# Kernel optimization log

Measured on AMD Instinct MI355X. Metric: run time of the kernel, lower is better.

## Reference

```python
import jax, jax.numpy as jnp
import numpy as np

B, NUM_GENES, F = 8, 20000, 128
N, E, H = 50000, 800000, 128


def setup_inputs() -> dict:
    key = jax.random.key(0)
    k = jax.random.split(key, 8)
    gene_emb = jax.random.normal(k[0], (B, NUM_GENES, F), dtype=jnp.float32)
    W1 = jax.random.normal(k[1], (F, H), dtype=jnp.float32) * 0.05
    b1 = jnp.zeros((H,), dtype=jnp.float32)
    W2 = jax.random.normal(k[2], (H, H), dtype=jnp.float32) * 0.05
    b2 = jnp.zeros((H,), dtype=jnp.float32)
    global_ids = jax.random.randint(k[3], (N,), 0, NUM_GENES, dtype=jnp.int64)
    edge_index = jax.random.randint(k[4], (2, E), 0, N, dtype=jnp.int64)
    return {"gene_emb": gene_emb, "W1": W1, "b1": b1, "W2": W2, "b2": b2,
            "global_ids": global_ids, "edge_index": edge_index}


def reference(gene_emb, W1, b1, W2, b2, global_ids, edge_index):
    n = global_ids.shape[0]
    # GCN normalization with self-loops (PyG GCNConv default):
    # A_hat = A + I, deg over target nodes, norm = d^{-1/2}[src] * d^{-1/2}[dst]
    loop = jnp.arange(n)
    src = jnp.concatenate([edge_index[0], loop])  # [E+N]
    dst = jnp.concatenate([edge_index[1], loop])  # [E+N]
    deg = jnp.zeros((n,), gene_emb.dtype).at[dst].add(1.0)
    dinv = jax.lax.rsqrt(deg)  # deg >= 1 thanks to self-loops
    norm = (dinv[src] * dinv[dst])[None, :, None]  # [1, E+N, 1]

    def gcn(x, W, b):
        h = x @ W                                   # [B, N, H] transform first (linear commutes)
        msg = h[:, src, :] * norm                   # gather + scale: [B, E+N, H]
        agg = jnp.zeros_like(h).at[:, dst].add(msg)  # scatter-add over targets
        return agg + b

    x = gene_emb[:, global_ids, :]                  # [B, N, F] node feature gather
    x = jax.nn.relu(gcn(x, W1, b1))
    x = gcn(x, W2, b2)
    # global_mean_pool: each batch replica is one whole graph -> mean over nodes
    return x.mean(axis=1)                           # [B, H]
```

## Files before the change

### kernel.cpp

```cpp
#include <hip/hip_runtime.h>

#define NG 20000
#define BB 8
#define FD 128

typedef unsigned int uint;
typedef unsigned short ushort;
typedef __attribute__((ext_vector_type(8))) short short8v;
typedef __attribute__((ext_vector_type(4))) float float4v;
typedef __attribute__((ext_vector_type(4))) int int4v;
typedef __attribute__((ext_vector_type(2))) float f2v;

__device__ f2v llvm_rbl_v2f32(int4v srsrc, int voffset, int soffset, int aux)
    __asm("llvm.amdgcn.raw.buffer.load.v2f32");

__device__ __forceinline__ int4v make_srsrc(const void* p) {
    int4v r;
    r.x = (int)(uint)(uintptr_t)p;
    r.y = (int)(uint)((uintptr_t)p >> 32);
    r.z = -1;
    r.w = 0x00020000;
    return r;
}

__device__ __forceinline__ ushort f2bf(float x) {
    uint u = __float_as_uint(x);
    u += 0x7FFFu + ((u >> 16) & 1u);
    return (ushort)(u >> 16);
}
__device__ __forceinline__ float bf_lo(uint u) { return __uint_as_float(u << 16); }
__device__ __forceinline__ float bf_hi(uint u) { return __uint_as_float(u & 0xFFFF0000u); }

__global__ void k_setup(int4* csrz, int zn4, int* ideg, float* s_acc,
                        const float* __restrict__ W1, ushort* w1t, int N) {
    int i = blockIdx.x * blockDim.x + threadIdx.x;
    if (i < zn4) csrz[i] = make_int4(0, 0, 0, 0);
    if (i < N) ideg[i] = 0;
    if (i < BB * FD) s_acc[i] = 0.0f;
    if (i < FD * FD) {
        int j = i >> 7, k = i & 127;
        w1t[i] = f2bf(W1[k * 128 + j]);
    }
}

__global__ void k_count(const int* __restrict__ dst, int* ideg, int E) {
    int e = blockIdx.x * blockDim.x + threadIdx.x;
    if (e < E) atomicAdd(&ideg[dst[e]], 1);
}

__global__ void k_scanA(const int* __restrict__ ideg, float* dinv, float* cval,
                        float* wself, int* padcnt, int* offs, int* bsums, int N) {
    __shared__ int sd[256];
    int t = threadIdx.x, idx = blockIdx.x * 256 + t;
    int v = 0;
    if (idx < N) {
        int d = ideg[idx] + 1;
        float fd = (float)d;
        dinv[idx]  = rsqrtf(fd);
        float iv = 1.0f / fd;
        cval[idx]  = iv;
        wself[idx] = iv;
        v = (d + 7) & ~7;
        padcnt[idx] = v;
    }
    sd[t] = v; __syncthreads();
    for (int o = 1; o < 256; o <<= 1) {
        int x = (t >= o) ? sd[t - o] : 0;
        __syncthreads();
        sd[t] += x;
        __syncthreads();
    }
    if (idx < N) offs[idx] = sd[t] - v;
    if (t == 255) bsums[blockIdx.x] = sd[255];
}

__global__ void k_scan2(int* bsums, int nb) {
    __shared__ int sd[256];
    int t = threadIdx.x;
    int v = (t < nb) ? bsums[t] : 0;
    sd[t] = v; __syncthreads();
    for (int o = 1; o < 256; o <<= 1) {
        int x = (t >= o) ? sd[t - o] : 0;
        __syncthreads();
        sd[t] += x;
        __syncthreads();
    }
    if (t < nb) bsums[t] = sd[t] - v;
}

__global__ void k_scanB(int* offs, const int* __restrict__ bsums,
                        const int* __restrict__ gid, const float* __restrict__ wself,
                        int* cursor, int2* csr, int N) {
    int i = blockIdx.x * blockDim.x + threadIdx.x;
    if (i < N) {
        int o = offs[i] + bsums[blockIdx.x];
        offs[i] = o;
        csr[o] = make_int2(gid[i], __float_as_int(wself[i]));
        cursor[i] = 1;
    }
}

__global__ __launch_bounds__(256, 3)
void k_fillh(const int* __restrict__ src, const int* __restrict__ dst,
             const int* __restrict__ gid, const float* __restrict__ dinv,
             float* cval, const int* __restrict__ offs, int* cursor,
             int2* csr, int E, int eb,
             const float* __restrict__ gene, const ushort* __restrict__ w1t,
             uint* __restrict__ h2u) {
    __shared__ __align__(16) char smem[49152];
    if ((int)blockIdx.x < eb) {
        int e = blockIdx.x * 256 + threadIdx.x;
        if (e >= E) return;
        int s = src[e], d = dst[e];
        float nrm = dinv[s] * dinv[d];
        atomicAdd(&cval[s], nrm);
        int pos = atomicAdd(&cursor[d], 1);
        csr[offs[d] + pos] = make_int2(gid[s], __float_as_int(nrm));
        return;
    }
    ushort* Al = (ushort*)smem;
    ushort* Bl = (ushort*)(smem + 16384);
    float*  Cl = (float*)smem;
    int t = threadIdx.x;
    int hb   = blockIdx.x - eb;
    int p    = hb & 3;
    int tile = hb >> 2;
    int g0   = tile * 32;

#pragma unroll
    for (int s = 0; s < 8; s++) {
        int f = t + s * 256;
        int r = f >> 5, k0 = (f & 31) * 4;
        int bb = 2 * p + (r >> 5);
        int gg = g0 + (r & 31);
        float4 v = *(const float4*)(gene + ((size_t)bb * NG + gg) * 128 + k0);
        ushort4 u;
        u.x = f2bf(v.x); u.y = f2bf(v.y); u.z = f2bf(v.z); u.w = f2bf(v.w);
        int byte = (r * 256 + k0 * 2) ^ ((r & 7) << 4);
        *(ushort4*)((char*)Al + byte) = u;
    }
#pragma unroll
    for (int s = 0; s < 8; s++) {
        int f = t + s * 256;
        int j = f >> 4, k0 = (f & 15) * 8;
        uint4 v = *(const uint4*)(w1t + j * 128 + k0);
        int byte = (j * 256 + k0 * 2) ^ ((j & 7) << 4);
        *(uint4*)((char*)Bl + byte) = v;
    }
    __syncthreads();

    int wid = t >> 6, lane = t & 63;
    int r0 = wid * 16;
    int lrow = lane & 15, lhi = lane >> 4;
    float4v acc[8];
#pragma unroll
    for (int nf = 0; nf < 8; nf++) acc[nf] = (float4v)(0.f);

#pragma unroll
    for (int c = 0; c < 4; c++) {
        int ra = r0 + lrow;
        int byteA = (ra * 256 + (c * 32 + lhi * 8) * 2) ^ ((ra & 7) << 4);
        short8v a = *(short8v*)((char*)Al + byteA);
#pragma unroll
        for (int nf = 0; nf < 8; nf++) {
            int jb = nf * 16 + lrow;
            int byteB = (jb * 256 + (c * 32 + lhi * 8) * 2) ^ ((jb & 7) << 4);
            short8v b = *(short8v*)((char*)Bl + byteB);
            acc[nf] = __builtin_amdgcn_mfma_f32_16x16x32_bf16(a, b, acc[nf], 0, 0, 0);
        }
    }
    __syncthreads();

#pragma unroll
    for (int nf = 0; nf < 8; nf++) {
#pragma unroll
        for (int q = 0; q < 4; q++) {
            Cl[(r0 + lhi * 4 + q) * 128 + nf * 16 + lrow] = acc[nf][q];
        }
    }
    __syncthreads();

#pragma unroll
    for (int s = 0; s < 16; s++) {
        int flat = t + s * 256;
        int gi = flat >> 7, cc = flat & 127;
        float lo = Cl[gi * 128 + cc];
        float hi = Cl[(32 + gi) * 128 + cc];
        uint u = (uint)f2bf(lo) | ((uint)f2bf(hi) << 16);
        h2u[((size_t)p * NG + g0 + gi) * 128 + cc] = u;
    }
}

__global__ __launch_bounds__(512)
void k_aggp(const uint* __restrict__ hp, const int2* __restrict__ csr,
            const int* __restrict__ offs, const int* __restrict__ padcnt,
            const float* __restrict__ cval, const float* __restrict__ b1,
            float* __restrict__ s_acc, int N, int npw) {
    int p    = blockIdx.x & 3;
    int wid  = threadIdx.x >> 6, lane = threadIdx.x & 63;
    int w    = __builtin_amdgcn_readfirstlane((blockIdx.x >> 2) * 8 + wid);
    int4v sr = make_srsrc(hp + (size_t)p * NG * 128);
    int voff = lane * 8;
    int l2 = lane * 2;
    float bx = b1[l2], by = b1[l2 + 1];
    float sx0 = 0.f, sx1 = 0.f, sy0 = 0.f, sy1 = 0.f;

    int i0 = w * npw;
    int i1 = min(N, i0 + npw);
    for (int i = i0; i < i1; ++i) {
        int   e  = offs[i];
        int   pc = padcnt[i];
        float cv = cval[i];
        float ax0 = 0.f, ax1 = 0.f, ay0 = 0.f, ay1 = 0.f;
        for (int q = 0; q < pc; q += 8) {
            int ee = e + q;
            int2 c0 = csr[ee],     c1 = csr[ee + 1], c2 = csr[ee + 2], c3 = csr[ee + 3];
            int2 c4 = csr[ee + 4], c5 = csr[ee + 5], c6 = csr[ee + 6], c7 = csr[ee + 7];
            f2v u0 = llvm_rbl_v2f32(sr, voff, c0.x << 9, 0);
            f2v u1 = llvm_rbl_v2f32(sr, voff, c1.x << 9, 0);
            f2v u2 = llvm_rbl_v2f32(sr, voff, c2.x << 9, 0);
            f2v u3 = llvm_rbl_v2f32(sr, voff, c3.x << 9, 0);
            f2v u4 = llvm_rbl_v2f32(sr, voff, c4.x << 9, 0);
            f2v u5 = llvm_rbl_v2f32(sr, voff, c5.x << 9, 0);
            f2v u6 = llvm_rbl_v2f32(sr, voff, c6.x << 9, 0);
            f2v u7 = llvm_rbl_v2f32(sr, voff, c7.x << 9, 0);
            float n0 = __int_as_float(c0.y), n1 = __int_as_float(c1.y);
            float n2 = __int_as_float(c2.y), n3 = __int_as_float(c3.y);
            float n4 = __int_as_float(c4.y), n5 = __int_as_float(c5.y);
            float n6 = __int_as_float(c6.y), n7 = __int_as_float(c7.y);
            uint a, b;
            a = __float_as_uint(u0.x); b = __float_as_uint(u0.y);
            ax0 = fmaf(n0, bf_lo(a), ax0); ax1 = fmaf(n0, bf_hi(a), ax1);
            ay0 = fmaf(n0, bf_lo(b), ay0); ay1 = fmaf(n0, bf_hi(b), ay1);
            a = __float_as_uint(u1.x); b = __float_as_uint(u1.y);
            ax0 = fmaf(n1, bf_lo(a), ax0); ax1 = fmaf(n1, bf_hi(a), ax1);
            ay0 = fmaf(n1, bf_lo(b), ay0); ay1 = fmaf(n1, bf_hi(b), ay1);
            a = __float_as_uint(u2.x); b = __float_as_uint(u2.y);
            ax0 = fmaf(n2, bf_lo(a), ax0); ax1 = fmaf(n2, bf_hi(a), ax1);
            ay0 = fmaf(n2, bf_lo(b), ay0); ay1 = fmaf(n2, bf_hi(b), ay1);
            a = __float_as_uint(u3.x); b = __float_as_uint(u3.y);
            ax0 = fmaf(n3, bf_lo(a), ax0); ax1 = fmaf(n3, bf_hi(a), ax1);
            ay0 = fmaf(n3, bf_lo(b), ay0); ay1 = fmaf(n3, bf_hi(b), ay1);
            a = __float_as_uint(u4.x); b = __float_as_uint(u4.y);
            ax0 = fmaf(n4, bf_lo(a), ax0); ax1 = fmaf(n4, bf_hi(a), ax1);
            ay0 = fmaf(n4, bf_lo(b), ay0); ay1 = fmaf(n4, bf_hi(b), ay1);
            a = __float_as_uint(u5.x); b = __float_as_uint(u5.y);
            ax0 = fmaf(n5, bf_lo(a), ax0); ax1 = fmaf(n5, bf_hi(a), ax1);
            ay0 = fmaf(n5, bf_lo(b), ay0); ay1 = fmaf(n5, bf_hi(b), ay1);
            a = __float_as_uint(u6.x); b = __float_as_uint(u6.y);
            ax0 = fmaf(n6, bf_lo(a), ax0); ax1 = fmaf(n6, bf_hi(a), ax1);
            ay0 = fmaf(n6, bf_lo(b), ay0); ay1 = fmaf(n6, bf_hi(b), ay1);
            a = __float_as_uint(u7.x); b = __float_as_uint(u7.y);
            ax0 = fmaf(n7, bf_lo(a), ax0); ax1 = fmaf(n7, bf_hi(a), ax1);
            ay0 = fmaf(n7, bf_lo(b), ay0); ay1 = fmaf(n7, bf_hi(b), ay1);
        }
        sx0 += cv * fmaxf(ax0 + bx, 0.f);
        sx1 += cv * fmaxf(ax1 + bx, 0.f);
        sy0 += cv * fmaxf(ay0 + by, 0.f);
        sy1 += cv * fmaxf(ay1 + by, 0.f);
    }

    __shared__ float red[8][256];
    red[wid][lane * 4 + 0] = sx0;
    red[wid][lane * 4 + 1] = sx1;
    red[wid][lane * 4 + 2] = sy0;
    red[wid][lane * 4 + 3] = sy1;
    __syncthreads();
    int t = threadIdx.x;
    if (t < 256) {
        float s = 0.f;
#pragma unroll
        for (int wv = 0; wv < 8; wv++) s += red[wv][t];
        int l = t >> 2, c = t & 3;
        atomicAdd(&s_acc[(2 * p + (c & 1)) * 128 + 2 * l + (c >> 1)], s);
    }
}

__global__ void k_final(const float* __restrict__ s_acc, const float* __restrict__ W2,
                        const float* __restrict__ b2, float* __restrict__ out, float invN) {
    __shared__ float ss[1024];
    int t = threadIdx.x;
    for (int idx = t; idx < 1024; idx += 128) ss[idx] = s_acc[idx];
    __syncthreads();
    float acc[8];
#pragma unroll
    for (int b = 0; b < 8; b++) acc[b] = 0.f;
    for (int k = 0; k < 128; k++) {
        float w = W2[k * 128 + t];
#pragma unroll
        for (int b = 0; b < 8; b++) acc[b] += ss[b * 128 + k] * w;
    }
    float bb = b2[t];
#pragma unroll
    for (int b = 0; b < 8; b++) out[b * 128 + t] = acc[b] * invN + bb;
}


extern "C" void kernel_launch(void* const* d_in, const int* in_sizes, int n_in,
                              void* d_out, int out_size, void* d_ws, size_t ws_size,
                              hipStream_t stream) {
    const float* gene = (const float*)d_in[0];
    const float* W1   = (const float*)d_in[1];
    const float* b1   = (const float*)d_in[2];
    const float* W2   = (const float*)d_in[3];
    const float* b2   = (const float*)d_in[4];
    const int*   gid  = (const int*)d_in[5];
    const int*   eidx = (const int*)d_in[6];
    int N = in_sizes[5];
    int E = in_sizes[6] / 2;
    const int* src = eidx;
    const int* dst = eidx + E;
    float* out = (float*)d_out;

    char* p = (char*)d_ws;
    auto alloc = [&](size_t bytes) -> char* {
        char* r = p; p += (bytes + 255) & ~(size_t)255; return r;
    };
    size_t csr_cap = (size_t)E + 8 * (size_t)N;
    int*   ideg   = (int*)  alloc((size_t)N * 4);
    float* dinv   = (float*)alloc((size_t)N * 4);
    float* cval   = (float*)alloc((size_t)N * 4);
    float* wself  = (float*)alloc((size_t)N * 4);
    int*   padcnt = (int*)  alloc((size_t)N * 4);
    int*   offs   = (int*)  alloc((size_t)N * 4);
    int*   cursor = (int*)  alloc((size_t)N * 4);
    int*   bsums  = (int*)  alloc(256 * 4);
    int2*  csr    = (int2*) alloc(csr_cap * 8);
    float* s_acc  = (float*)alloc(1024 * 4);
    uint*  h2     = (uint*) alloc((size_t)NG * BB * FD * 2);
    ushort* w1t   = (ushort*)alloc(128 * 128 * 2);

    int nb = (N + 255) / 256;
    int eb = (E + 255) / 256;
    int zn4 = (int)(csr_cap * 8 / 16);
    int zb  = (zn4 + 255) / 256;
    int hblk = 4 * (NG / 32);

    const int NBLK = 2048;
    int wavesPerPair = (NBLK / 4) * 8;
    int npw = (N + wavesPerPair - 1) / wavesPerPair;

    k_setup<<<zb, 256, 0, stream>>>((int4*)csr, zn4, ideg, s_acc, W1, w1t, N);
    k_count<<<eb, 256, 0, stream>>>(dst, ideg, E);
    k_scanA<<<nb, 256, 0, stream>>>(ideg, dinv, cval, wself, padcnt, offs, bsums, N);
    k_scan2<<<1, 256, 0, stream>>>(bsums, nb);
    k_scanB<<<nb, 256, 0, stream>>>(offs, bsums, gid, wself, cursor, csr, N);
    k_fillh<<<eb + hblk, 256, 0, stream>>>(src, dst, gid, dinv, cval, offs, cursor,
                                           csr, E, eb, gene, w1t, h2);
    k_aggp <<<NBLK, 512, 0, stream>>>(h2, csr, offs, padcnt,
                                      cval, b1, s_acc, N, npw);
    k_final<<<1, 128, 0, stream>>>(s_acc, W2, b2, out, 1.0f / (float)N);
}
```

Measured before the change: 306.6 us.

## Fuse CSR build phases into one persistent kernel with grid barriers

Merges count, scan, scan-add, and edge-fill kernels into a single persistent kernel of 256 blocks that uses atomic grid barriers between phases. The remaining 256 blocks run the X@W1 MFMA tiles in a grid-stride loop concurrently with the graph build. The full CSR zero-fill is replaced by zeroing only the padding slots per node, and the s_acc atomics are spread over 8 replicas that k_final sums. The aim is to cut launch overhead, the large memset, and atomic contention. The cost is spin-wait barriers that rely on all 512 blocks being co-resident.

```diff
diff --git a/kernel.cpp b/kernel.cpp
--- a/kernel.cpp
+++ b/kernel.cpp
@@ -3,6 +3,8 @@
 #define NG 20000
 #define BB 8
 #define FD 128
+#define NBT 512
+#define NBS 256
 
 typedef unsigned int uint;
 typedef unsigned short ushort;
@@ -31,163 +33,168 @@
 __device__ __forceinline__ float bf_lo(uint u) { return __uint_as_float(u << 16); }
 __device__ __forceinline__ float bf_hi(uint u) { return __uint_as_float(u & 0xFFFF0000u); }
 
-__global__ void k_setup(int4* csrz, int zn4, int* ideg, float* s_acc,
+__global__ void k_setup(int* ideg, float* s_acc, uint* bar,
                         const float* __restrict__ W1, ushort* w1t, int N) {
     int i = blockIdx.x * blockDim.x + threadIdx.x;
-    if (i < zn4) csrz[i] = make_int4(0, 0, 0, 0);
     if (i < N) ideg[i] = 0;
-    if (i < BB * FD) s_acc[i] = 0.0f;
+    if (i < 8 * BB * FD) s_acc[i] = 0.0f;
+    if (i < 4) bar[i] = 0u;
     if (i < FD * FD) {
         int j = i >> 7, k = i & 127;
         w1t[i] = f2bf(W1[k * 128 + j]);
     }
 }
 
-__global__ void k_count(const int* __restrict__ dst, int* ideg, int E) {
-    int e = blockIdx.x * blockDim.x + threadIdx.x;
-    if (e < E) atomicAdd(&ideg[dst[e]], 1);
-}
-
-__global__ void k_scanA(const int* __restrict__ ideg, float* dinv, float* cval,
-                        float* wself, int* padcnt, int* offs, int* bsums, int N) {
-    __shared__ int sd[256];
-    int t = threadIdx.x, idx = blockIdx.x * 256 + t;
-    int v = 0;
-    if (idx < N) {
-        int d = ideg[idx] + 1;
-        float fd = (float)d;
-        dinv[idx]  = rsqrtf(fd);
-        float iv = 1.0f / fd;
-        cval[idx]  = iv;
-        wself[idx] = iv;
-        v = (d + 7) & ~7;
-        padcnt[idx] = v;
-    }
-    sd[t] = v; __syncthreads();
-    for (int o = 1; o < 256; o <<= 1) {
-        int x = (t >= o) ? sd[t - o] : 0;
-        __syncthreads();
-        sd[t] += x;
-        __syncthreads();
-    }
-    if (idx < N) offs[idx] = sd[t] - v;
-    if (t == 255) bsums[blockIdx.x] = sd[255];
-}
-
-__global__ void k_scan2(int* bsums, int nb) {
-    __shared__ int sd[256];
-    int t = threadIdx.x;
-    int v = (t < nb) ? bsums[t] : 0;
-    sd[t] = v; __syncthreads();
-    for (int o = 1; o < 256; o <<= 1) {
-        int x = (t >= o) ? sd[t - o] : 0;
-        __syncthreads();
-        sd[t] += x;
-        __syncthreads();
-    }
-    if (t < nb) bsums[t] = sd[t] - v;
-}
-
-__global__ void k_scanB(int* offs, const int* __restrict__ bsums,
-                        const int* __restrict__ gid, const float* __restrict__ wself,
-                        int* cursor, int2* csr, int N) {
-    int i = blockIdx.x * blockDim.x + threadIdx.x;
-    if (i < N) {
-        int o = offs[i] + bsums[blockIdx.x];
-        offs[i] = o;
-        csr[o] = make_int2(gid[i], __float_as_int(wself[i]));
-        cursor[i] = 1;
-    }
-}
-
-__global__ __launch_bounds__(256, 3)
-void k_fillh(const int* __restrict__ src, const int* __restrict__ dst,
-             const int* __restrict__ gid, const float* __restrict__ dinv,
-             float* cval, const int* __restrict__ offs, int* cursor,
-             int2* csr, int E, int eb,
+__device__ __forceinline__ void gbar(uint* bar, int ph) {
+    __syncthreads();
+    if (threadIdx.x == 0) {
+        __threadfence();
+        atomicAdd(&bar[ph], 1u);
+        while (atomicAdd(&bar[ph], 0u) < (uint)NBS) __builtin_amdgcn_s_sleep(4);
+    }
+    __syncthreads();
+    __threadfence();
+}
+
+__global__ __launch_bounds__(256)
+void k_build(const int* __restrict__ src, const int* __restrict__ dst,
+             const int* __restrict__ gid, int E, int N, int nb,
+             int* ideg, float* dinv, float* cval, int* padcnt, int* offs,
+             int* cursor, int2* csr, int* bsums, uint* bar,
              const float* __restrict__ gene, const ushort* __restrict__ w1t,
              uint* __restrict__ h2u) {
     __shared__ __align__(16) char smem[49152];
-    if ((int)blockIdx.x < eb) {
-        int e = blockIdx.x * 256 + threadIdx.x;
-        if (e >= E) return;
-        int s = src[e], d = dst[e];
-        float nrm = dinv[s] * dinv[d];
+    int bid = blockIdx.x, t = threadIdx.x;
+
+    if (bid >= NBS) {
+        ushort* Al = (ushort*)smem;
+        ushort* Bl = (ushort*)(smem + 16384);
+        float*  Cl = (float*)smem;
+        int ntile = 4 * (NG / 32);
+        for (int tile = bid - NBS; tile < ntile; tile += (NBT - NBS)) {
+            int p = tile & 3, g0 = (tile >> 2) * 32;
+#pragma unroll
+            for (int s = 0; s < 8; s++) {
+                int f = t + s * 256;
+                int r = f >> 5, k0 = (f & 31) * 4;
+                int bb = 2 * p + (r >> 5);
+                int gg = g0 + (r & 31);
+                float4 v = *(const float4*)(gene + ((size_t)bb * NG + gg) * 128 + k0);
+                ushort4 u;
+                u.x = f2bf(v.x); u.y = f2bf(v.y); u.z = f2bf(v.z); u.w = f2bf(v.w);
+                int byte = (r * 256 + k0 * 2) ^ ((r & 7) << 4);
+                *(ushort4*)((char*)Al + byte) = u;
+            }
+#pragma unroll
+            for (int s = 0; s < 8; s++) {
+                int f = t + s * 256;
+                int j = f >> 4, k0 = (f & 15) * 8;
+                uint4 v = *(const uint4*)(w1t + j * 128 + k0);
+                int byte = (j * 256 + k0 * 2) ^ ((j & 7) << 4);
+                *(uint4*)((char*)Bl + byte) = v;
+            }
+            __syncthreads();
+
+            int wid = t >> 6, lane = t & 63;
+            int r0 = wid * 16;
+            int lrow = lane & 15, lhi = lane >> 4;
+            float4v acc[8];
+#pragma unroll
+            for (int nf = 0; nf < 8; nf++) acc[nf] = (float4v)(0.f);
+#pragma unroll
+            for (int c = 0; c < 4; c++) {
+                int ra = r0 + lrow;
+                int byteA = (ra * 256 + (c * 32 + lhi * 8) * 2) ^ ((ra & 7) << 4);
+                short8v a = *(short8v*)((char*)Al + byteA);
+#pragma unroll
+                for (int nf = 0; nf < 8; nf++) {
+                    int jb = nf * 16 + lrow;
+                    int byteB = (jb * 256 + (c * 32 + lhi * 8) * 2) ^ ((jb & 7) << 4);
+                    short8v b = *(short8v*)((char*)Bl + byteB);
+                    acc[nf] = __builtin_amdgcn_mfma_f32_16x16x32_bf16(a, b, acc[nf], 0, 0, 0);
+                }
+            }
+            __syncthreads();
+#pragma unroll
+            for (int nf = 0; nf < 8; nf++) {
+#pragma unroll
+                for (int q = 0; q < 4; q++) {
+                    Cl[(r0 + lhi * 4 + q) * 128 + nf * 16 + lrow] = acc[nf][q];
+                }
+            }
+            __syncthreads();
+#pragma unroll
+            for (int s = 0; s < 16; s++) {
+                int flat = t + s * 256;
+                int gi = flat >> 7, cc = flat & 127;
+                float lo = Cl[gi * 128 + cc];
+                float hi = Cl[(32 + gi) * 128 + cc];
+                uint u = (uint)f2bf(lo) | ((uint)f2bf(hi) << 16);
+                h2u[((size_t)p * NG + g0 + gi) * 128 + cc] = u;
+            }
+            __syncthreads();
+        }
+        return;
+    }
+
+    int* sd = (int*)smem;
+
+    for (int e = bid * 256 + t; e < E; e += NBS * 256)
+        atomicAdd(&ideg[dst[e]], 1);
+    gbar(bar, 0);
+
+    int idx = bid * 256 + t;
+    int v = 0, d = 0, off_part = 0;
+    float iv = 0.f;
+    if (bid < nb) {
+        if (idx < N) {
+            d = ideg[idx] + 1;
+            float fd = (float)d;
+            dinv[idx] = rsqrtf(fd);
+            iv = 1.0f / fd;
+            cval[idx] = iv;
+            v = (d + 7) & ~7;
+            padcnt[idx] = v;
+        }
+        sd[t] = v; __syncthreads();
+        for (int o = 1; o < 256; o <<= 1) {
+            int x = (t >= o) ? sd[t - o] : 0;
+            __syncthreads();
+            sd[t] += x;
+            __syncthreads();
+        }
+        off_part = sd[t] - v;
+        if (t == 255) bsums[bid] = sd[255];
+    }
+    gbar(bar, 1);
+
+    if (bid < nb) {
+        int v2 = (t < nb) ? bsums[t] : 0;
+        __syncthreads();
+        sd[t] = v2; __syncthreads();
+        for (int o = 1; o < 256; o <<= 1) {
+            int x = (t >= o) ? sd[t - o] : 0;
+            __syncthreads();
+            sd[t] += x;
+            __syncthreads();
+        }
+        int prefix = (bid > 0) ? sd[bid - 1] : 0;
+        if (idx < N) {
+            int o = off_part + prefix;
+            offs[idx] = o;
+            csr[o] = make_int2(gid[idx], __float_as_int(iv));
+            cursor[idx] = 1;
+            for (int z = d; z < v; z++) csr[o + z] = make_int2(0, 0);
+        }
+    }
+    gbar(bar, 2);
+
+    for (int e = bid * 256 + t; e < E; e += NBS * 256) {
+        int s = src[e], dd = dst[e];
+        float nrm = dinv[s] * dinv[dd];
         atomicAdd(&cval[s], nrm);
-        int pos = atomicAdd(&cursor[d], 1);
-        csr[offs[d] + pos] = make_int2(gid[s], __float_as_int(nrm));
-        return;
-    }
-    ushort* Al = (ushort*)smem;
-    ushort* Bl = (ushort*)(smem + 16384);
-    float*  Cl = (float*)smem;
-    int t = threadIdx.x;
-    int hb   = blockIdx.x - eb;
-    int p    = hb & 3;
-    int tile = hb >> 2;
-    int g0   = tile * 32;
-
-#pragma unroll
-    for (int s = 0; s < 8; s++) {
-        int f = t + s * 256;
-        int r = f >> 5, k0 = (f & 31) * 4;
-        int bb = 2 * p + (r >> 5);
-        int gg = g0 + (r & 31);
-        float4 v = *(const float4*)(gene + ((size_t)bb * NG + gg) * 128 + k0);
-        ushort4 u;
-        u.x = f2bf(v.x); u.y = f2bf(v.y); u.z = f2bf(v.z); u.w = f2bf(v.w);
-        int byte = (r * 256 + k0 * 2) ^ ((r & 7) << 4);
-        *(ushort4*)((char*)Al + byte) = u;
-    }
-#pragma unroll
-    for (int s = 0; s < 8; s++) {
-        int f = t + s * 256;
-        int j = f >> 4, k0 = (f & 15) * 8;
-        uint4 v = *(const uint4*)(w1t + j * 128 + k0);
-        int byte = (j * 256 + k0 * 2) ^ ((j & 7) << 4);
-        *(uint4*)((char*)Bl + byte) = v;
-    }
-    __syncthreads();
-
-    int wid = t >> 6, lane = t & 63;
-    int r0 = wid * 16;
-    int lrow = lane & 15, lhi = lane >> 4;
-    float4v acc[8];
-#pragma unroll
-    for (int nf = 0; nf < 8; nf++) acc[nf] = (float4v)(0.f);
-
-#pragma unroll
-    for (int c = 0; c < 4; c++) {
-        int ra = r0 + lrow;
-        int byteA = (ra * 256 + (c * 32 + lhi * 8) * 2) ^ ((ra & 7) << 4);
-        short8v a = *(short8v*)((char*)Al + byteA);
-#pragma unroll
-        for (int nf = 0; nf < 8; nf++) {
-            int jb = nf * 16 + lrow;
-            int byteB = (jb * 256 + (c * 32 + lhi * 8) * 2) ^ ((jb & 7) << 4);
-            short8v b = *(short8v*)((char*)Bl + byteB);
-            acc[nf] = __builtin_amdgcn_mfma_f32_16x16x32_bf16(a, b, acc[nf], 0, 0, 0);
-        }
-    }
-    __syncthreads();
-
-#pragma unroll
-    for (int nf = 0; nf < 8; nf++) {
-#pragma unroll
-        for (int q = 0; q < 4; q++) {
-            Cl[(r0 + lhi * 4 + q) * 128 + nf * 16 + lrow] = acc[nf][q];
-        }
-    }
-    __syncthreads();
-
-#pragma unroll
-    for (int s = 0; s < 16; s++) {
-        int flat = t + s * 256;
-        int gi = flat >> 7, cc = flat & 127;
-        float lo = Cl[gi * 128 + cc];
-        float hi = Cl[(32 + gi) * 128 + cc];
-        uint u = (uint)f2bf(lo) | ((uint)f2bf(hi) << 16);
-        h2u[((size_t)p * NG + g0 + gi) * 128 + cc] = u;
+        int pos = atomicAdd(&cursor[dd], 1);
+        csr[offs[dd] + pos] = make_int2(gid[s], __float_as_int(nrm));
     }
 }
 
@@ -272,7 +279,8 @@
 #pragma unroll
         for (int wv = 0; wv < 8; wv++) s += red[wv][t];
         int l = t >> 2, c = t & 3;
-        atomicAdd(&s_acc[(2 * p + (c & 1)) * 128 + 2 * l + (c >> 1)], s);
+        int rep = (blockIdx.x >> 2) & 7;
+        atomicAdd(&s_acc[rep * 1024 + (2 * p + (c & 1)) * 128 + 2 * l + (c >> 1)], s);
     }
 }
 
@@ -280,7 +288,12 @@
                         const float* __restrict__ b2, float* __restrict__ out, float invN) {
     __shared__ float ss[1024];
     int t = threadIdx.x;
-    for (int idx = t; idx < 1024; idx += 128) ss[idx] = s_acc[idx];
+    for (int idx = t; idx < 1024; idx += 128) {
+        float s = 0.f;
+#pragma unroll
+        for (int r = 0; r < 8; r++) s += s_acc[r * 1024 + idx];
+        ss[idx] = s;
+    }
     __syncthreads();
     float acc[8];
 #pragma unroll
@@ -320,33 +333,26 @@
     int*   ideg   = (int*)  alloc((size_t)N * 4);
     float* dinv   = (float*)alloc((size_t)N * 4);
     float* cval   = (float*)alloc((size_t)N * 4);
-    float* wself  = (float*)alloc((size_t)N * 4);
     int*   padcnt = (int*)  alloc((size_t)N * 4);
     int*   offs   = (int*)  alloc((size_t)N * 4);
     int*   cursor = (int*)  alloc((size_t)N * 4);
     int*   bsums  = (int*)  alloc(256 * 4);
+    uint*  bar    = (uint*) alloc(64 * 4);
     int2*  csr    = (int2*) alloc(csr_cap * 8);
-    float* s_acc  = (float*)alloc(1024 * 4);
+    float* s_acc  = (float*)alloc(8 * 1024 * 4);
     uint*  h2     = (uint*) alloc((size_t)NG * BB * FD * 2);
     ushort* w1t   = (ushort*)alloc(128 * 128 * 2);
 
     int nb = (N + 255) / 256;
-    int eb = (E + 255) / 256;
-    int zn4 = (int)(csr_cap * 8 / 16);
-    int zb  = (zn4 + 255) / 256;
-    int hblk = 4 * (NG / 32);
 
     const int NBLK = 2048;
     int wavesPerPair = (NBLK / 4) * 8;
     int npw = (N + wavesPerPair - 1) / wavesPerPair;
 
-    k_setup<<<zb, 256, 0, stream>>>((int4*)csr, zn4, ideg, s_acc, W1, w1t, N);
-    k_count<<<eb, 256, 0, stream>>>(dst, ideg, E);
-    k_scanA<<<nb, 256, 0, stream>>>(ideg, dinv, cval, wself, padcnt, offs, bsums, N);
-    k_scan2<<<1, 256, 0, stream>>>(bsums, nb);
-    k_scanB<<<nb, 256, 0, stream>>>(offs, bsums, gid, wself, cursor, csr, N);
-    k_fillh<<<eb + hblk, 256, 0, stream>>>(src, dst, gid, dinv, cval, offs, cursor,
-                                           csr, E, eb, gene, w1t, h2);
+    k_setup<<<nb, 256, 0, stream>>>(ideg, s_acc, bar, W1, w1t, N);
+    k_build<<<NBT, 256, 0, stream>>>(src, dst, gid, E, N, nb,
+                                     ideg, dinv, cval, padcnt, offs, cursor, csr,
+                                     bsums, bar, gene, w1t, h2);
     k_aggp <<<NBLK, 512, 0, stream>>>(h2, csr, offs, padcnt,
                                       cval, b1, s_acc, N, npw);
     k_final<<<1, 128, 0, stream>>>(s_acc, W2, b2, out, 1.0f / (float)N);
```

Result: slower. 411.5 us (+34.2%).

## Zero only CSR padding slots, merge block-scan kernels, replicate pooled accumulators

Applied to the files above, without the earlier changes.

Drops the full-buffer zeroing of the CSR array in setup; instead each node zeroes only its own padding slots after its degree-rounded segment is placed. It folds the single-block scan of block sums into scanB, so each block recomputes its prefix, and it drops the wself buffer by recomputing 1/deg inline. The pooled accumulator is replicated 8 ways to cut atomic contention in k_aggp, with k_final summing the replicas. Node ranges per wave are now split evenly rather than by ceiling division. Together these remove a large memory write and a launch, at the cost of a redundant per-block scan and a serial padding loop per node.

```diff
diff --git a/kernel.cpp b/kernel.cpp
--- a/kernel.cpp
+++ b/kernel.cpp
@@ -31,12 +31,11 @@
 __device__ __forceinline__ float bf_lo(uint u) { return __uint_as_float(u << 16); }
 __device__ __forceinline__ float bf_hi(uint u) { return __uint_as_float(u & 0xFFFF0000u); }
 
-__global__ void k_setup(int4* csrz, int zn4, int* ideg, float* s_acc,
+__global__ void k_setup(int* ideg, float* s_acc,
                         const float* __restrict__ W1, ushort* w1t, int N) {
     int i = blockIdx.x * blockDim.x + threadIdx.x;
-    if (i < zn4) csrz[i] = make_int4(0, 0, 0, 0);
     if (i < N) ideg[i] = 0;
-    if (i < BB * FD) s_acc[i] = 0.0f;
+    if (i < 8 * BB * FD) s_acc[i] = 0.0f;
     if (i < FD * FD) {
         int j = i >> 7, k = i & 127;
         w1t[i] = f2bf(W1[k * 128 + j]);
@@ -49,17 +48,15 @@
 }
 
 __global__ void k_scanA(const int* __restrict__ ideg, float* dinv, float* cval,
-                        float* wself, int* padcnt, int* offs, int* bsums, int N) {
+                        int* padcnt, int* offs, int* bsums, int N) {
     __shared__ int sd[256];
     int t = threadIdx.x, idx = blockIdx.x * 256 + t;
     int v = 0;
     if (idx < N) {
         int d = ideg[idx] + 1;
         float fd = (float)d;
-        dinv[idx]  = rsqrtf(fd);
-        float iv = 1.0f / fd;
-        cval[idx]  = iv;
-        wself[idx] = iv;
+        dinv[idx] = rsqrtf(fd);
+        cval[idx] = 1.0f / fd;
         v = (d + 7) & ~7;
         padcnt[idx] = v;
     }
@@ -74,7 +71,10 @@
     if (t == 255) bsums[blockIdx.x] = sd[255];
 }
 
-__global__ void k_scan2(int* bsums, int nb) {
+__global__ void k_scanB(int* offs, const int* __restrict__ bsums,
+                        const int* __restrict__ ideg, const int* __restrict__ padcnt,
+                        const int* __restrict__ gid,
+                        int* cursor, int2* csr, int N, int nb) {
     __shared__ int sd[256];
     int t = threadIdx.x;
     int v = (t < nb) ? bsums[t] : 0;
@@ -85,18 +85,18 @@
         sd[t] += x;
         __syncthreads();
     }
-    if (t < nb) bsums[t] = sd[t] - v;
-}
-
-__global__ void k_scanB(int* offs, const int* __restrict__ bsums,
-                        const int* __restrict__ gid, const float* __restrict__ wself,
-                        int* cursor, int2* csr, int N) {
-    int i = blockIdx.x * blockDim.x + threadIdx.x;
+    int bid = blockIdx.x;
+    int prefix = (bid > 0) ? sd[bid - 1] : 0;
+    int i = bid * 256 + t;
     if (i < N) {
-        int o = offs[i] + bsums[blockIdx.x];
+        int o = offs[i] + prefix;
         offs[i] = o;
-        csr[o] = make_int2(gid[i], __float_as_int(wself[i]));
+        int d  = ideg[i] + 1;
+        int v8 = padcnt[i];
+        float iv = 1.0f / (float)d;
+        csr[o] = make_int2(gid[i], __float_as_int(iv));
         cursor[i] = 1;
+        for (int z = d; z < v8; z++) csr[o + z] = make_int2(0, 0);
     }
 }
 
@@ -195,7 +195,7 @@
 void k_aggp(const uint* __restrict__ hp, const int2* __restrict__ csr,
             const int* __restrict__ offs, const int* __restrict__ padcnt,
             const float* __restrict__ cval, const float* __restrict__ b1,
-            float* __restrict__ s_acc, int N, int npw) {
+            float* __restrict__ s_acc, int N, int wpp) {
     int p    = blockIdx.x & 3;
     int wid  = threadIdx.x >> 6, lane = threadIdx.x & 63;
     int w    = __builtin_amdgcn_readfirstlane((blockIdx.x >> 2) * 8 + wid);
@@ -205,8 +205,8 @@
     float bx = b1[l2], by = b1[l2 + 1];
     float sx0 = 0.f, sx1 = 0.f, sy0 = 0.f, sy1 = 0.f;
 
-    int i0 = w * npw;
-    int i1 = min(N, i0 + npw);
+    int i0 = (int)((long long)w * N / wpp);
+    int i1 = (int)((long long)(w + 1) * N / wpp);
     for (int i = i0; i < i1; ++i) {
         int   e  = offs[i];
         int   pc = padcnt[i];
@@ -272,7 +272,8 @@
 #pragma unroll
         for (int wv = 0; wv < 8; wv++) s += red[wv][t];
         int l = t >> 2, c = t & 3;
-        atomicAdd(&s_acc[(2 * p + (c & 1)) * 128 + 2 * l + (c >> 1)], s);
+        int rep = (blockIdx.x >> 2) & 7;
+        atomicAdd(&s_acc[rep * 1024 + (2 * p + (c & 1)) * 128 + 2 * l + (c >> 1)], s);
     }
 }
 
@@ -280,7 +281,12 @@
                         const float* __restrict__ b2, float* __restrict__ out, float invN) {
     __shared__ float ss[1024];
     int t = threadIdx.x;
-    for (int idx = t; idx < 1024; idx += 128) ss[idx] = s_acc[idx];
+    for (int idx = t; idx < 1024; idx += 128) {
+        float s = 0.f;
+#pragma unroll
+        for (int r = 0; r < 8; r++) s += s_acc[r * 1024 + idx];
+        ss[idx] = s;
+    }
     __syncthreads();
     float acc[8];
 #pragma unroll
@@ -320,34 +326,29 @@
     int*   ideg   = (int*)  alloc((size_t)N * 4);
     float* dinv   = (float*)alloc((size_t)N * 4);
     float* cval   = (float*)alloc((size_t)N * 4);
-    float* wself  = (float*)alloc((size_t)N * 4);
     int*   padcnt = (int*)  alloc((size_t)N * 4);
     int*   offs   = (int*)  alloc((size_t)N * 4);
     int*   cursor = (int*)  alloc((size_t)N * 4);
     int*   bsums  = (int*)  alloc(256 * 4);
     int2*  csr    = (int2*) alloc(csr_cap * 8);
-    float* s_acc  = (float*)alloc(1024 * 4);
+    float* s_acc  = (float*)alloc(8 * 1024 * 4);
     uint*  h2     = (uint*) alloc((size_t)NG * BB * FD * 2);
     ushort* w1t   = (ushort*)alloc(128 * 128 * 2);
 
     int nb = (N + 255) / 256;
     int eb = (E + 255) / 256;
-    int zn4 = (int)(csr_cap * 8 / 16);
-    int zb  = (zn4 + 255) / 256;
     int hblk = 4 * (NG / 32);
 
     const int NBLK = 2048;
-    int wavesPerPair = (NBLK / 4) * 8;
-    int npw = (N + wavesPerPair - 1) / wavesPerPair;
-
-    k_setup<<<zb, 256, 0, stream>>>((int4*)csr, zn4, ideg, s_acc, W1, w1t, N);
+    int wpp = (NBLK / 4) * 8;
+
+    k_setup<<<nb, 256, 0, stream>>>(ideg, s_acc, W1, w1t, N);
     k_count<<<eb, 256, 0, stream>>>(dst, ideg, E);
-    k_scanA<<<nb, 256, 0, stream>>>(ideg, dinv, cval, wself, padcnt, offs, bsums, N);
-    k_scan2<<<1, 256, 0, stream>>>(bsums, nb);
-    k_scanB<<<nb, 256, 0, stream>>>(offs, bsums, gid, wself, cursor, csr, N);
+    k_scanA<<<nb, 256, 0, stream>>>(ideg, dinv, cval, padcnt, offs, bsums, N);
+    k_scanB<<<nb, 256, 0, stream>>>(offs, bsums, ideg, padcnt, gid, cursor, csr, N, nb);
     k_fillh<<<eb + hblk, 256, 0, stream>>>(src, dst, gid, dinv, cval, offs, cursor,
                                            csr, E, eb, gene, w1t, h2);
     k_aggp <<<NBLK, 512, 0, stream>>>(h2, csr, offs, padcnt,
-                                      cval, b1, s_acc, N, npw);
+                                      cval, b1, s_acc, N, wpp);
     k_final<<<1, 128, 0, stream>>>(s_acc, W2, b2, out, 1.0f / (float)N);
 }
```

Result: no change. 304.0 us (-0.9%).
